# Optimization experiments

Hardware: AMD Instinct MI355X
Metric: run time of the kernel (lower is better)

Reference implementation:

```python
import jax, jax.numpy as jnp
import numpy as np

B, S, D, DFF = 4, 2048, 1024, 4096
EPS = 1e-5


def layernorm(x, g, b):
    mu = jnp.mean(x, axis=-1, keepdims=True)
    var = jnp.mean(jnp.square(x - mu), axis=-1, keepdims=True)
    return (x - mu) * jax.lax.rsqrt(var + EPS) * g + b


def setup_inputs() -> dict:
    key = jax.random.key(0)
    ks = jax.random.split(key, 4)
    hidden_state = jax.random.normal(ks[0], (B, S, D), dtype=jnp.float32)
    attention_mask = jnp.zeros((B, 1, S), dtype=jnp.float32)  # additive mask
    w1 = jax.random.normal(ks[1], (D, DFF), dtype=jnp.float32) * (1.0 / np.sqrt(D))
    b1 = jnp.zeros((DFF,), dtype=jnp.float32)
    w2 = jax.random.normal(ks[2], (DFF, D), dtype=jnp.float32) * (1.0 / np.sqrt(DFF))
    b2 = jnp.zeros((D,), dtype=jnp.float32)
    ln1_g = jnp.ones((D,), dtype=jnp.float32)
    ln1_b = jnp.zeros((D,), dtype=jnp.float32)
    ln2_g = jnp.ones((D,), dtype=jnp.float32)
    ln2_b = jnp.zeros((D,), dtype=jnp.float32)
    return dict(hidden_state=hidden_state, attention_mask=attention_mask,
                w1=w1, b1=b1, w2=w2, b2=b2,
                ln1_g=ln1_g, ln1_b=ln1_b, ln2_g=ln2_g, ln2_b=ln2_b)


def reference(hidden_state, attention_mask, w1, b1, w2, b2, ln1_g, ln1_b, ln2_g, ln2_b):
    x = hidden_state
    d = jnp.asarray(x.shape[-1], x.dtype)
    # hand-rolled single-head attention: q=k=v=x (source forward ignores QKV projections)
    scores = jnp.einsum('bqd,bkd->bqk', x, x) / jnp.sqrt(d) + attention_mask  # [B,S,S]
    attn = jax.nn.softmax(scores, axis=-1)
    attn_out = jnp.einsum('bqk,bkd->bqd', attn, x)
    h = layernorm(x + attn_out, ln1_g, ln1_b)
    # FFN: dense -> exact GELU -> linear_2
    ffn = jnp.einsum('bsf,fd->bsd', jax.nn.gelu(jnp.einsum('bsd,df->bsf', h, w1) + b1, approximate=False), w2) + b2
    return layernorm(h + ffn, ln2_g, ln2_b)
```

## Files before the change

### kernel.cpp

```cpp
#include <hip/hip_runtime.h>
#include <hip/hip_bf16.h>
#include <math.h>

#define LN_EPS 1e-5f

typedef short short8 __attribute__((ext_vector_type(8)));
typedef float floatx4 __attribute__((ext_vector_type(4)));

__device__ inline unsigned short f2bf(float f) {
    unsigned int u = __float_as_uint(f);
    u += 0x7fff + ((u >> 16) & 1);
    return (unsigned short)(u >> 16);
}

__device__ inline void gl_lds16(const unsigned short* g, unsigned short* l) {
    __builtin_amdgcn_global_load_lds(
        (__attribute__((address_space(1))) const void*)g,
        (__attribute__((address_space(3))) void*)l, 16, 0, 0);
}

__device__ inline float gelu_f(float v) {
    float u2 = 2.0f * v * (0.7978845608f + 0.0356774081f * v * v);
    float t  = 1.0f - 2.0f / (__expf(u2) + 1.0f);
    return 0.5f * v * (1.0f + t);
}

#define CFENCE asm volatile("" ::: "memory")

template<int EPI, int BN>
__global__ __launch_bounds__(512, 2) void gemm8p(
    const unsigned short* __restrict__ A, const unsigned short* __restrict__ B,
    const float* __restrict__ bias, const float* __restrict__ resid,
    void* __restrict__ Cptr,
    int M, int N, int K, long sA, long sB, long sC, long sBias, float scale)
{
    static_assert(BN == 256 || BN == 128, "BN must be 256 or 128");
    constexpr int WC = BN / 4;
    constexpr int NT = WC / 16;
    constexpr int NH = NT / 2;

    __shared__ alignas(16) unsigned short lds_a[2][2][256 * 32];
    __shared__ alignas(16) unsigned short lds_b[2][2][BN * 32];

    const int tid  = threadIdx.x;
    const int lane = tid & 63;
    const int wave = tid >> 6;
    const int quad = lane >> 4;
    const int l16  = lane & 15;
    const int wm = wave >> 2;
    const int wn = wave & 3;

    const int nwg = gridDim.x * gridDim.y * gridDim.z;
    int lin = blockIdx.x + gridDim.x * (blockIdx.y + gridDim.y * blockIdx.z);
    if ((nwg & 7) == 0) lin = (lin & 7) * (nwg >> 3) + (lin >> 3);
    const int bx = lin % gridDim.x;
    const int byz = lin / gridDim.x;
    const int by = byz % gridDim.y;
    const int bz = byz / gridDim.y;

    const int tile_m = by * 256;
    const int tile_n = bx * BN;
    const int batch  = bz;

    const unsigned short* Ab = A + (size_t)batch * sA;
    const unsigned short* Bb = B + (size_t)batch * sB;

    const int srow = tid >> 2;
    const int scs  = ((tid & 3) ^ ((tid & 32) ? 2 : 0)) * 8;
    const unsigned short* gA = Ab + (size_t)(tile_m + srow) * K + scs;
    const unsigned short* gB = Bb + (size_t)(tile_n + srow) * K + scs;
    const int ldst = tid * 8;

    const int kcs   = (quad * 8) ^ ((l16 & 8) << 1);
    const int abase = (wm * 128 + l16) * 32 + kcs;
    const int bbase = (wn * WC  + l16) * 32 + kcs;

    floatx4 acc[8][NT];
    const floatx4 zero = {0.f, 0.f, 0.f, 0.f};
#pragma unroll
    for (int i = 0; i < 8; i++)
#pragma unroll
        for (int j = 0; j < NT; j++) acc[i][j] = zero;

    auto stageA = [&](int buf, int h, int k0) {
        const unsigned short* s = gA + (size_t)h * 128 * K + k0;
        gl_lds16(s,      &lds_a[buf][0][h * 4096 + ldst]);
        gl_lds16(s + 32, &lds_a[buf][1][h * 4096 + ldst]);
    };
    auto stageB = [&](int buf, int h, int k0) {
        const unsigned short* s = gB + (size_t)h * 128 * K + k0;
        gl_lds16(s,      &lds_b[buf][0][h * 4096 + ldst]);
        gl_lds16(s + 32, &lds_b[buf][1][h * 4096 + ldst]);
    };

    const int nt = K >> 6;

    stageA(0, 0, 0); stageA(0, 1, 0);
    stageB(0, 0, 0);
    if constexpr (BN == 256) stageB(0, 1, 0);
    if (nt > 1) {
        stageB(1, 0, 64);
        if constexpr (BN == 256) stageB(1, 1, 64);
        if constexpr (BN == 256) { asm volatile("s_waitcnt vmcnt(4)" ::: "memory"); }
        else                     { asm volatile("s_waitcnt vmcnt(2)" ::: "memory"); }
    } else {
        asm volatile("s_waitcnt vmcnt(0)" ::: "memory");
    }
    __builtin_amdgcn_s_barrier(); CFENCE;

    int cur = 0;

    if constexpr (BN == 128) {
        for (int t = 0; t < nt; ++t) {
            const int k0 = t * 64;
            short8 afr[4][2], bfr[2][2];

#pragma unroll
            for (int i = 0; i < 4; i++)
#pragma unroll
                for (int kh = 0; kh < 2; kh++)
                    afr[i][kh] = *(const short8*)&lds_a[cur][kh][abase + i * 512];
#pragma unroll
            for (int j = 0; j < 2; j++)
#pragma unroll
                for (int kh = 0; kh < 2; kh++)
                    bfr[j][kh] = *(const short8*)&lds_b[cur][kh][bbase + j * 512];
            if (t + 1 < nt) { stageA(cur ^ 1, 0, k0 + 64); stageA(cur ^ 1, 1, k0 + 64); }
            CFENCE; __builtin_amdgcn_s_barrier(); CFENCE;
            __builtin_amdgcn_s_setprio(1);
#pragma unroll
            for (int i = 0; i < 4; i++)
#pragma unroll
                for (int j = 0; j < 2; j++)
#pragma unroll
                    for (int kh = 0; kh < 2; kh++)
                        acc[i][j] = __builtin_amdgcn_mfma_f32_16x16x32_bf16(
                            bfr[j][kh], afr[i][kh], acc[i][j], 0, 0, 0);
            __builtin_amdgcn_s_setprio(0);
            CFENCE; __builtin_amdgcn_s_barrier(); CFENCE;

#pragma unroll
            for (int i = 0; i < 4; i++)
#pragma unroll
                for (int kh = 0; kh < 2; kh++)
                    afr[i][kh] = *(const short8*)&lds_a[cur][kh][abase + (4 + i) * 512];
            if (t + 2 < nt) stageB(cur, 0, k0 + 128);
            __builtin_amdgcn_s_setprio(1);
#pragma unroll
            for (int i = 0; i < 4; i++)
#pragma unroll
                for (int j = 0; j < 2; j++)
#pragma unroll
                    for (int kh = 0; kh < 2; kh++)
                        acc[4 + i][j] = __builtin_amdgcn_mfma_f32_16x16x32_bf16(
                            bfr[j][kh], afr[i][kh], acc[4 + i][j], 0, 0, 0);
            __builtin_amdgcn_s_setprio(0);
            if (t + 3 <= nt) {
                asm volatile("s_waitcnt vmcnt(2)" ::: "memory");
                __builtin_amdgcn_s_barrier(); CFENCE;
            } else if (t + 2 == nt) {
                asm volatile("s_waitcnt vmcnt(0)" ::: "memory");
                __builtin_amdgcn_s_barrier(); CFENCE;
            }
            cur ^= 1;
        }
    } else {
        for (int t = 0; t < nt; ++t) {
            const int k0 = t * 64;
            short8 afr[4][2], bfrA[NH][2], bfrB[NH][2];

#pragma unroll
            for (int i = 0; i < 4; i++)
#pragma unroll
                for (int kh = 0; kh < 2; kh++)
                    afr[i][kh] = *(const short8*)&lds_a[cur][kh][abase + i * 512];
#pragma unroll
            for (int j = 0; j < NH; j++)
#pragma unroll
                for (int kh = 0; kh < 2; kh++)
                    bfrA[j][kh] = *(const short8*)&lds_b[cur][kh][bbase + j * 512];
            if (t + 1 < nt) stageA(cur ^ 1, 0, k0 + 64);
            CFENCE; __builtin_amdgcn_s_barrier(); CFENCE;
            __builtin_amdgcn_s_setprio(1);
#pragma unroll
            for (int i = 0; i < 4; i++)
#pragma unroll
                for (int j = 0; j < NH; j++)
#pragma unroll
                    for (int kh = 0; kh < 2; kh++)
                        acc[i][j] = __builtin_amdgcn_mfma_f32_16x16x32_bf16(
                            bfrA[j][kh], afr[i][kh], acc[i][j], 0, 0, 0);
            __builtin_amdgcn_s_setprio(0);
            CFENCE; __builtin_amdgcn_s_barrier(); CFENCE;

#pragma unroll
            for (int j = 0; j < NH; j++)
#pragma unroll
                for (int kh = 0; kh < 2; kh++)
                    bfrB[j][kh] = *(const short8*)&lds_b[cur][kh][bbase + (NH + j) * 512];
            if (t + 1 < nt) stageA(cur ^ 1, 1, k0 + 64);
            CFENCE; __builtin_amdgcn_s_barrier(); CFENCE;
            __builtin_amdgcn_s_setprio(1);
#pragma unroll
            for (int i = 0; i < 4; i++)
#pragma unroll
                for (int j = 0; j < NH; j++)
#pragma unroll
                    for (int kh = 0; kh < 2; kh++)
                        acc[i][NH + j] = __builtin_amdgcn_mfma_f32_16x16x32_bf16(
                            bfrB[j][kh], afr[i][kh], acc[i][NH + j], 0, 0, 0);
            __builtin_amdgcn_s_setprio(0);
            CFENCE; __builtin_amdgcn_s_barrier(); CFENCE;

#pragma unroll
            for (int i = 0; i < 4; i++)
#pragma unroll
                for (int kh = 0; kh < 2; kh++)
                    afr[i][kh] = *(const short8*)&lds_a[cur][kh][abase + (4 + i) * 512];
            if (t + 2 < nt) stageB(cur, 0, k0 + 128);
            CFENCE; __builtin_amdgcn_s_barrier(); CFENCE;
            __builtin_amdgcn_s_setprio(1);
#pragma unroll
            for (int i = 0; i < 4; i++)
#pragma unroll
                for (int j = 0; j < NH; j++)
#pragma unroll
                    for (int kh = 0; kh < 2; kh++)
                        acc[4 + i][NH + j] = __builtin_amdgcn_mfma_f32_16x16x32_bf16(
                            bfrB[j][kh], afr[i][kh], acc[4 + i][NH + j], 0, 0, 0);
            __builtin_amdgcn_s_setprio(0);
            CFENCE; __builtin_amdgcn_s_barrier(); CFENCE;

            if (t + 2 < nt) stageB(cur, 1, k0 + 128);
            __builtin_amdgcn_s_setprio(1);
#pragma unroll
            for (int i = 0; i < 4; i++)
#pragma unroll
                for (int j = 0; j < NH; j++)
#pragma unroll
                    for (int kh = 0; kh < 2; kh++)
                        acc[4 + i][j] = __builtin_amdgcn_mfma_f32_16x16x32_bf16(
                            bfrA[j][kh], afr[i][kh], acc[4 + i][j], 0, 0, 0);
            __builtin_amdgcn_s_setprio(0);
            if (t + 3 <= nt) {
                asm volatile("s_waitcnt vmcnt(4)" ::: "memory");
                __builtin_amdgcn_s_barrier(); CFENCE;
            } else if (t + 2 == nt) {
                asm volatile("s_waitcnt vmcnt(0)" ::: "memory");
                __builtin_amdgcn_s_barrier(); CFENCE;
            }
            cur ^= 1;
        }
    }

#pragma unroll
    for (int i = 0; i < 8; i++) {
        const int row = tile_m + wm * 128 + i * 16 + l16;
#pragma unroll
        for (int j = 0; j < NT; j++) {
            const int colb = tile_n + wn * WC + j * 16 + quad * 4;
            float v[4];
#pragma unroll
            for (int r = 0; r < 4; r++) v[r] = acc[i][j][r];

            if (EPI == 3) {
                float4 mv = *(const float4*)&bias[(size_t)batch * sBias + colb];
                v[0] = v[0] * scale + mv.x;  v[1] = v[1] * scale + mv.y;
                v[2] = v[2] * scale + mv.z;  v[3] = v[3] * scale + mv.w;
            }
            if (EPI == 2 || EPI == 5) {
                float4 bv = *(const float4*)&bias[colb];
                v[0] += bv.x; v[1] += bv.y; v[2] += bv.z; v[3] += bv.w;
            }
            if (EPI == 2) {
#pragma unroll
                for (int r = 0; r < 4; r++) v[r] = gelu_f(v[r]);
            }
            if (EPI == 4 || EPI == 5) {
                float4 rv = *(const float4*)&resid[(size_t)batch * sC +
                                                   (size_t)row * N + colb];
                v[0] += rv.x; v[1] += rv.y; v[2] += rv.z; v[3] += rv.w;
            }

            if (EPI == 2 || EPI == 3) {
                unsigned short* C = (unsigned short*)Cptr + (size_t)batch * sC;
                ushort4 h4;
                h4.x = f2bf(v[0]); h4.y = f2bf(v[1]);
                h4.z = f2bf(v[2]); h4.w = f2bf(v[3]);
                *(ushort4*)(C + (size_t)row * N + colb) = h4;
            } else {
                float* C = (float*)Cptr + (size_t)batch * sC;
                float4 f4 = {v[0], v[1], v[2], v[3]};
                *(float4*)(C + (size_t)row * N + colb) = f4;
            }
        }
    }
}

__global__ __launch_bounds__(256) void x_prep_kernel(
    const float* __restrict__ in, unsigned short* __restrict__ straight,
    unsigned short* __restrict__ transposed, int R, int C, long sIn)
{
    __shared__ float tile[32][33];
    const int tc = blockIdx.x * 32, tr = blockIdx.y * 32;
    const float* src = in + (size_t)blockIdx.z * sIn;
    unsigned short* dstS = straight   + (size_t)blockIdx.z * sIn;
    unsigned short* dstT = transposed + (size_t)blockIdx.z * sIn;
    const int tx = threadIdx.x & 31, ty = threadIdx.x >> 5;
#pragma unroll
    for (int i = 0; i < 4; i++) {
        float val = src[(size_t)(tr + ty + i * 8) * C + tc + tx];
        tile[ty + i * 8][tx] = val;
        dstS[(size_t)(tr + ty + i * 8) * C + tc + tx] = f2bf(val);
    }
    __syncthreads();
#pragma unroll
    for (int i = 0; i < 4; i++)
        dstT[(size_t)(tc + ty + i * 8) * R + tr + tx] = f2bf(tile[tx][ty + i * 8]);
}

__global__ __launch_bounds__(256) void transpose_cvt_kernel(
    const float* __restrict__ in, unsigned short* __restrict__ out, int R, int C)
{
    __shared__ float tile[32][33];
    const int tc = blockIdx.x * 32, tr = blockIdx.y * 32;
    const int tx = threadIdx.x & 31, ty = threadIdx.x >> 5;
#pragma unroll
    for (int i = 0; i < 4; i++)
        tile[ty + i * 8][tx] = in[(size_t)(tr + ty + i * 8) * C + tc + tx];
    __syncthreads();
#pragma unroll
    for (int i = 0; i < 4; i++)
        out[(size_t)(tc + ty + i * 8) * R + tr + tx] = f2bf(tile[tx][ty + i * 8]);
}

__global__ __launch_bounds__(256) void softmax_bf16_kernel(
    const unsigned short* __restrict__ scores, unsigned short* __restrict__ probs,
    int S)
{
    __shared__ float red[4];
    const int row = blockIdx.x;
    const unsigned short* p = scores + (size_t)row * S;
    unsigned short* pr      = probs  + (size_t)row * S;
    const int tid  = threadIdx.x;
    const int lane = tid & 63;
    const int wav  = tid >> 6;

    uint4 raw = *(const uint4*)(p + tid * 8);
    float v[8];
    v[0] = __uint_as_float(raw.x << 16); v[1] = __uint_as_float(raw.x & 0xffff0000u);
    v[2] = __uint_as_float(raw.y << 16); v[3] = __uint_as_float(raw.y & 0xffff0000u);
    v[4] = __uint_as_float(raw.z << 16); v[5] = __uint_as_float(raw.z & 0xffff0000u);
    v[6] = __uint_as_float(raw.w << 16); v[7] = __uint_as_float(raw.w & 0xffff0000u);

    float mx = v[0];
#pragma unroll
    for (int k = 1; k < 8; k++) mx = fmaxf(mx, v[k]);
#pragma unroll
    for (int off = 32; off > 0; off >>= 1) mx = fmaxf(mx, __shfl_down(mx, off));
    if (lane == 0) red[wav] = mx;
    __syncthreads();
    mx = fmaxf(fmaxf(red[0], red[1]), fmaxf(red[2], red[3]));
    __syncthreads();

    float s = 0.f;
#pragma unroll
    for (int k = 0; k < 8; k++) { v[k] = __expf(v[k] - mx); s += v[k]; }
#pragma unroll
    for (int off = 32; off > 0; off >>= 1) s += __shfl_down(s, off);
    if (lane == 0) red[wav] = s;
    __syncthreads();
    s = red[0] + red[1] + red[2] + red[3];
    float inv = 1.0f / s;

    uint4 o;
    o.x = (unsigned)f2bf(v[0] * inv) | ((unsigned)f2bf(v[1] * inv) << 16);
    o.y = (unsigned)f2bf(v[2] * inv) | ((unsigned)f2bf(v[3] * inv) << 16);
    o.z = (unsigned)f2bf(v[4] * inv) | ((unsigned)f2bf(v[5] * inv) << 16);
    o.w = (unsigned)f2bf(v[6] * inv) | ((unsigned)f2bf(v[7] * inv) << 16);
    *(uint4*)(pr + tid * 8) = o;
}

template<int WRITE_BF16>
__global__ __launch_bounds__(256) void ln_kernel(
    const float* __restrict__ X,
    const float* __restrict__ g, const float* __restrict__ bta,
    float* __restrict__ out, unsigned short* __restrict__ out16, int D)
{
    __shared__ float red[8];
    const int row = blockIdx.x;
    const float* x = X + (size_t)row * D;
    const int tid  = threadIdx.x;
    const int lane = tid & 63;
    const int wav  = tid >> 6;

    float4 a = *(const float4*)(x + tid * 4);
    float v0 = a.x, v1 = a.y, v2 = a.z, v3 = a.w;

    float s1 = v0 + v1 + v2 + v3;
    float s2 = v0 * v0 + v1 * v1 + v2 * v2 + v3 * v3;
#pragma unroll
    for (int off = 32; off > 0; off >>= 1) {
        s1 += __shfl_down(s1, off);
        s2 += __shfl_down(s2, off);
    }
    if (lane == 0) { red[wav] = s1; red[4 + wav] = s2; }
    __syncthreads();
    s1 = red[0] + red[1] + red[2] + red[3];
    s2 = red[4] + red[5] + red[6] + red[7];
    const float mu  = s1 / (float)D;
    const float var = s2 / (float)D - mu * mu;
    const float rs  = rsqrtf(var + LN_EPS);

    float4 gg = *(const float4*)(g + tid * 4);
    float4 bb = *(const float4*)(bta + tid * 4);
    float4 r;
    r.x = (v0 - mu) * rs * gg.x + bb.x;
    r.y = (v1 - mu) * rs * gg.y + bb.y;
    r.z = (v2 - mu) * rs * gg.z + bb.z;
    r.w = (v3 - mu) * rs * gg.w + bb.w;
    *(float4*)(out + (size_t)row * D + tid * 4) = r;
    if (WRITE_BF16) {
        ushort4 h;
        h.x = f2bf(r.x); h.y = f2bf(r.y); h.z = f2bf(r.z); h.w = f2bf(r.w);
        *(ushort4*)(out16 + (size_t)row * D + tid * 4) = h;
    }
}

extern "C" void kernel_launch(void* const* d_in, const int* in_sizes, int n_in,
                              void* d_out, int out_size, void* d_ws, size_t ws_size,
                              hipStream_t stream) {
    (void)in_sizes; (void)n_in; (void)out_size; (void)ws_size;
    const float* x    = (const float*)d_in[0];
    const float* mask = (const float*)d_in[1];
    const float* w1   = (const float*)d_in[2];
    const float* b1   = (const float*)d_in[3];
    const float* w2   = (const float*)d_in[4];
    const float* b2   = (const float*)d_in[5];
    const float* ln1g = (const float*)d_in[6];
    const float* ln1b = (const float*)d_in[7];
    const float* ln2g = (const float*)d_in[8];
    const float* ln2b = (const float*)d_in[9];
    float* out = (float*)d_out;

    const int B = 4, S = 2048, D = 1024, DFF = 4096;
    const size_t MB = 1024 * 1024;

    char* ws = (char*)d_ws;
    unsigned short* scoresb = (unsigned short*)ws;
    unsigned short* act     = (unsigned short*)ws;
    unsigned short* xb      = (unsigned short*)(ws + 32 * MB);
    unsigned short* probs   = (unsigned short*)(ws + 32 * MB);
    float*          hbuf    = (float*)(ws + 64 * MB);
    unsigned short* hb16    = (unsigned short*)(ws + 96 * MB);
    unsigned short* w1T     = (unsigned short*)(ws + 112 * MB);
    unsigned short* w2T     = (unsigned short*)(ws + 120 * MB);
    unsigned short* xTb     = (unsigned short*)d_out;
    float*          fsum    = (float*)d_out;

    x_prep_kernel<<<dim3(D / 32, S / 32, B), 256, 0, stream>>>(
        x, xb, xTb, S, D, (long)S * D);
    transpose_cvt_kernel<<<dim3(DFF / 32, D / 32, 1), 256, 0, stream>>>(w1, w1T, D, DFF);
    transpose_cvt_kernel<<<dim3(D / 32, DFF / 32, 1), 256, 0, stream>>>(w2, w2T, DFF, D);

    hipLaunchKernelGGL((gemm8p<3, 256>), dim3(S / 256, S / 256, B), dim3(512), 0, stream,
                       xb, xb, mask, (const float*)nullptr, (void*)scoresb,
                       S, S, D, (long)S * D, (long)S * D, (long)S * S, (long)S, 0.03125f);
    softmax_bf16_kernel<<<B * S, 256, 0, stream>>>(scoresb, probs, S);
    hipLaunchKernelGGL((gemm8p<4, 128>), dim3(D / 128, S / 256, B), dim3(512), 0, stream,
                       probs, xTb, (const float*)nullptr, x, (void*)hbuf,
                       S, D, S, (long)S * S, (long)D * S, (long)S * D, 0L, 0.f);
    hipLaunchKernelGGL((ln_kernel<1>), dim3(B * S), dim3(256), 0, stream,
                       hbuf, ln1g, ln1b, hbuf, hb16, D);
    hipLaunchKernelGGL((gemm8p<2, 256>), dim3(DFF / 256, (B * S) / 256, 1), dim3(512), 0, stream,
                       hb16, w1T, b1, (const float*)nullptr, (void*)act,
                       B * S, DFF, D, 0L, 0L, 0L, 0L, 0.f);
    hipLaunchKernelGGL((gemm8p<5, 256>), dim3(D / 256, (B * S) / 256, 1), dim3(512), 0, stream,
                       act, w2T, b2, hbuf, (void*)fsum,
                       B * S, D, DFF, 0L, 0L, 0L, 0L, 0.f);
    hipLaunchKernelGGL((ln_kernel<0>), dim3(B * S), dim3(256), 0, stream,
                       fsum, ln2g, ln2b, out, (unsigned short*)nullptr, D);
}
```

Before: 455.7 us.

## Add 128x128 GEMM kernel for the N=1024 attention-output and FFN2 GEMMs

Adds a new 256-thread gemm128 kernel with 128x128 tiles and 4 waves, and uses it for the PV GEMM and the FFN second GEMM (N=1024, fp32 output with residual). The grids grow: FFN2 goes from 128 to 512 workgroups and PV from 256 to 512. The aim is better occupancy and load balance across the CUs for these narrow-N GEMMs. gemm8p is reduced to BN=256 with bf16 output only, and the cost is lower per-tile reuse in the new kernel, with more global and LDS traffic per FLOP.

Result: faster. 408.6 us (-10.3%).

```diff
diff --git a/kernel.cpp b/kernel.cpp
--- a/kernel.cpp
+++ b/kernel.cpp
@@ -34,7 +34,7 @@
     void* __restrict__ Cptr,
     int M, int N, int K, long sA, long sB, long sC, long sBias, float scale)
 {
-    static_assert(BN == 256 || BN == 128, "BN must be 256 or 128");
+    static_assert(BN == 256, "gemm8p: BN==256 only (BN=128 -> gemm128)");
     constexpr int WC = BN / 4;
     constexpr int NT = WC / 16;
     constexpr int NH = NT / 2;
@@ -96,161 +96,101 @@
     const int nt = K >> 6;
 
     stageA(0, 0, 0); stageA(0, 1, 0);
-    stageB(0, 0, 0);
-    if constexpr (BN == 256) stageB(0, 1, 0);
+    stageB(0, 0, 0); stageB(0, 1, 0);
     if (nt > 1) {
-        stageB(1, 0, 64);
-        if constexpr (BN == 256) stageB(1, 1, 64);
-        if constexpr (BN == 256) { asm volatile("s_waitcnt vmcnt(4)" ::: "memory"); }
-        else                     { asm volatile("s_waitcnt vmcnt(2)" ::: "memory"); }
+        stageB(1, 0, 64); stageB(1, 1, 64);
+        asm volatile("s_waitcnt vmcnt(4)" ::: "memory");
     } else {
         asm volatile("s_waitcnt vmcnt(0)" ::: "memory");
     }
     __builtin_amdgcn_s_barrier(); CFENCE;
 
     int cur = 0;
-
-    if constexpr (BN == 128) {
-        for (int t = 0; t < nt; ++t) {
-            const int k0 = t * 64;
-            short8 afr[4][2], bfr[2][2];
-
-#pragma unroll
-            for (int i = 0; i < 4; i++)
+    for (int t = 0; t < nt; ++t) {
+        const int k0 = t * 64;
+        short8 afr[4][2], bfrA[NH][2], bfrB[NH][2];
+
+#pragma unroll
+        for (int i = 0; i < 4; i++)
+#pragma unroll
+            for (int kh = 0; kh < 2; kh++)
+                afr[i][kh] = *(const short8*)&lds_a[cur][kh][abase + i * 512];
+#pragma unroll
+        for (int j = 0; j < NH; j++)
+#pragma unroll
+            for (int kh = 0; kh < 2; kh++)
+                bfrA[j][kh] = *(const short8*)&lds_b[cur][kh][bbase + j * 512];
+        if (t + 1 < nt) stageA(cur ^ 1, 0, k0 + 64);
+        CFENCE; __builtin_amdgcn_s_barrier(); CFENCE;
+        __builtin_amdgcn_s_setprio(1);
+#pragma unroll
+        for (int i = 0; i < 4; i++)
+#pragma unroll
+            for (int j = 0; j < NH; j++)
 #pragma unroll
                 for (int kh = 0; kh < 2; kh++)
-                    afr[i][kh] = *(const short8*)&lds_a[cur][kh][abase + i * 512];
-#pragma unroll
-            for (int j = 0; j < 2; j++)
+                    acc[i][j] = __builtin_amdgcn_mfma_f32_16x16x32_bf16(
+                        bfrA[j][kh], afr[i][kh], acc[i][j], 0, 0, 0);
+        __builtin_amdgcn_s_setprio(0);
+        CFENCE; __builtin_amdgcn_s_barrier(); CFENCE;
+
+#pragma unroll
+        for (int j = 0; j < NH; j++)
+#pragma unroll
+            for (int kh = 0; kh < 2; kh++)
+                bfrB[j][kh] = *(const short8*)&lds_b[cur][kh][bbase + (NH + j) * 512];
+        if (t + 1 < nt) stageA(cur ^ 1, 1, k0 + 64);
+        CFENCE; __builtin_amdgcn_s_barrier(); CFENCE;
+        __builtin_amdgcn_s_setprio(1);
+#pragma unroll
+        for (int i = 0; i < 4; i++)
+#pragma unroll
+            for (int j = 0; j < NH; j++)
 #pragma unroll
                 for (int kh = 0; kh < 2; kh++)
-                    bfr[j][kh] = *(const short8*)&lds_b[cur][kh][bbase + j * 512];
-            if (t + 1 < nt) { stageA(cur ^ 1, 0, k0 + 64); stageA(cur ^ 1, 1, k0 + 64); }
-            CFENCE; __builtin_amdgcn_s_barrier(); CFENCE;
-            __builtin_amdgcn_s_setprio(1);
-#pragma unroll
-            for (int i = 0; i < 4; i++)
-#pragma unroll
-                for (int j = 0; j < 2; j++)
-#pragma unroll
-                    for (int kh = 0; kh < 2; kh++)
-                        acc[i][j] = __builtin_amdgcn_mfma_f32_16x16x32_bf16(
-                            bfr[j][kh], afr[i][kh], acc[i][j], 0, 0, 0);
-            __builtin_amdgcn_s_setprio(0);
-            CFENCE; __builtin_amdgcn_s_barrier(); CFENCE;
-
-#pragma unroll
-            for (int i = 0; i < 4; i++)
+                    acc[i][NH + j] = __builtin_amdgcn_mfma_f32_16x16x32_bf16(
+                        bfrB[j][kh], afr[i][kh], acc[i][NH + j], 0, 0, 0);
+        __builtin_amdgcn_s_setprio(0);
+        CFENCE; __builtin_amdgcn_s_barrier(); CFENCE;
+
+#pragma unroll
+        for (int i = 0; i < 4; i++)
+#pragma unroll
+            for (int kh = 0; kh < 2; kh++)
+                afr[i][kh] = *(const short8*)&lds_a[cur][kh][abase + (4 + i) * 512];
+        if (t + 2 < nt) stageB(cur, 0, k0 + 128);
+        CFENCE; __builtin_amdgcn_s_barrier(); CFENCE;
+        __builtin_amdgcn_s_setprio(1);
+#pragma unroll
+        for (int i = 0; i < 4; i++)
+#pragma unroll
+            for (int j = 0; j < NH; j++)
 #pragma unroll
                 for (int kh = 0; kh < 2; kh++)
-                    afr[i][kh] = *(const short8*)&lds_a[cur][kh][abase + (4 + i) * 512];
-            if (t + 2 < nt) stageB(cur, 0, k0 + 128);
-            __builtin_amdgcn_s_setprio(1);
-#pragma unroll
-            for (int i = 0; i < 4; i++)
-#pragma unroll
-                for (int j = 0; j < 2; j++)
-#pragma unroll
-                    for (int kh = 0; kh < 2; kh++)
-                        acc[4 + i][j] = __builtin_amdgcn_mfma_f32_16x16x32_bf16(
-                            bfr[j][kh], afr[i][kh], acc[4 + i][j], 0, 0, 0);
-            __builtin_amdgcn_s_setprio(0);
-            if (t + 3 <= nt) {
-                asm volatile("s_waitcnt vmcnt(2)" ::: "memory");
-                __builtin_amdgcn_s_barrier(); CFENCE;
-            } else if (t + 2 == nt) {
-                asm volatile("s_waitcnt vmcnt(0)" ::: "memory");
-                __builtin_amdgcn_s_barrier(); CFENCE;
-            }
-            cur ^= 1;
+                    acc[4 + i][NH + j] = __builtin_amdgcn_mfma_f32_16x16x32_bf16(
+                        bfrB[j][kh], afr[i][kh], acc[4 + i][NH + j], 0, 0, 0);
+        __builtin_amdgcn_s_setprio(0);
+        CFENCE; __builtin_amdgcn_s_barrier(); CFENCE;
+
+        if (t + 2 < nt) stageB(cur, 1, k0 + 128);
+        __builtin_amdgcn_s_setprio(1);
+#pragma unroll
+        for (int i = 0; i < 4; i++)
+#pragma unroll
+            for (int j = 0; j < NH; j++)
+#pragma unroll
+                for (int kh = 0; kh < 2; kh++)
+                    acc[4 + i][j] = __builtin_amdgcn_mfma_f32_16x16x32_bf16(
+                        bfrA[j][kh], afr[i][kh], acc[4 + i][j], 0, 0, 0);
+        __builtin_amdgcn_s_setprio(0);
+        if (t + 3 <= nt) {
+            asm volatile("s_waitcnt vmcnt(4)" ::: "memory");
+            __builtin_amdgcn_s_barrier(); CFENCE;
+        } else if (t + 2 == nt) {
+            asm volatile("s_waitcnt vmcnt(0)" ::: "memory");
+            __builtin_amdgcn_s_barrier(); CFENCE;
         }
-    } else {
-        for (int t = 0; t < nt; ++t) {
-            const int k0 = t * 64;
-            short8 afr[4][2], bfrA[NH][2], bfrB[NH][2];
-
-#pragma unroll
-            for (int i = 0; i < 4; i++)
-#pragma unroll
-                for (int kh = 0; kh < 2; kh++)
-                    afr[i][kh] = *(const short8*)&lds_a[cur][kh][abase + i * 512];
-#pragma unroll
-            for (int j = 0; j < NH; j++)
-#pragma unroll
-                for (int kh = 0; kh < 2; kh++)
-                    bfrA[j][kh] = *(const short8*)&lds_b[cur][kh][bbase + j * 512];
-            if (t + 1 < nt) stageA(cur ^ 1, 0, k0 + 64);
-            CFENCE; __builtin_amdgcn_s_barrier(); CFENCE;
-            __builtin_amdgcn_s_setprio(1);
-#pragma unroll
-            for (int i = 0; i < 4; i++)
-#pragma unroll
-                for (int j = 0; j < NH; j++)
-#pragma unroll
-                    for (int kh = 0; kh < 2; kh++)
-                        acc[i][j] = __builtin_amdgcn_mfma_f32_16x16x32_bf16(
-                            bfrA[j][kh], afr[i][kh], acc[i][j], 0, 0, 0);
-            __builtin_amdgcn_s_setprio(0);
-            CFENCE; __builtin_amdgcn_s_barrier(); CFENCE;
-
-#pragma unroll
-            for (int j = 0; j < NH; j++)
-#pragma unroll
-                for (int kh = 0; kh < 2; kh++)
-                    bfrB[j][kh] = *(const short8*)&lds_b[cur][kh][bbase + (NH + j) * 512];
-            if (t + 1 < nt) stageA(cur ^ 1, 1, k0 + 64);
-            CFENCE; __builtin_amdgcn_s_barrier(); CFENCE;
-            __builtin_amdgcn_s_setprio(1);
-#pragma unroll
-            for (int i = 0; i < 4; i++)
-#pragma unroll
-                for (int j = 0; j < NH; j++)
-#pragma unroll
-                    for (int kh = 0; kh < 2; kh++)
-                        acc[i][NH + j] = __builtin_amdgcn_mfma_f32_16x16x32_bf16(
-                            bfrB[j][kh], afr[i][kh], acc[i][NH + j], 0, 0, 0);
-            __builtin_amdgcn_s_setprio(0);
-            CFENCE; __builtin_amdgcn_s_barrier(); CFENCE;
-
-#pragma unroll
-            for (int i = 0; i < 4; i++)
-#pragma unroll
-                for (int kh = 0; kh < 2; kh++)
-                    afr[i][kh] = *(const short8*)&lds_a[cur][kh][abase + (4 + i) * 512];
-            if (t + 2 < nt) stageB(cur, 0, k0 + 128);
-            CFENCE; __builtin_amdgcn_s_barrier(); CFENCE;
-            __builtin_amdgcn_s_setprio(1);
-#pragma unroll
-            for (int i = 0; i < 4; i++)
-#pragma unroll
-                for (int j = 0; j < NH; j++)
-#pragma unroll
-                    for (int kh = 0; kh < 2; kh++)
-                        acc[4 + i][NH + j] = __builtin_amdgcn_mfma_f32_16x16x32_bf16(
-                            bfrB[j][kh], afr[i][kh], acc[4 + i][NH + j], 0, 0, 0);
-            __builtin_amdgcn_s_setprio(0);
-            CFENCE; __builtin_amdgcn_s_barrier(); CFENCE;
-
-            if (t + 2 < nt) stageB(cur, 1, k0 + 128);
-            __builtin_amdgcn_s_setprio(1);
-#pragma unroll
-            for (int i = 0; i < 4; i++)
-#pragma unroll
-                for (int j = 0; j < NH; j++)
-#pragma unroll
-                    for (int kh = 0; kh < 2; kh++)
-                        acc[4 + i][j] = __builtin_amdgcn_mfma_f32_16x16x32_bf16(
-                            bfrA[j][kh], afr[i][kh], acc[4 + i][j], 0, 0, 0);
-            __builtin_amdgcn_s_setprio(0);
-            if (t + 3 <= nt) {
-                asm volatile("s_waitcnt vmcnt(4)" ::: "memory");
-                __builtin_amdgcn_s_barrier(); CFENCE;
-            } else if (t + 2 == nt) {
-                asm volatile("s_waitcnt vmcnt(0)" ::: "memory");
-                __builtin_amdgcn_s_barrier(); CFENCE;
-            }
-            cur ^= 1;
-        }
+        cur ^= 1;
     }
 
 #pragma unroll
@@ -268,31 +208,177 @@
                 v[0] = v[0] * scale + mv.x;  v[1] = v[1] * scale + mv.y;
                 v[2] = v[2] * scale + mv.z;  v[3] = v[3] * scale + mv.w;
             }
-            if (EPI == 2 || EPI == 5) {
+            if (EPI == 2) {
+                float4 bv = *(const float4*)&bias[colb];
+                v[0] += bv.x; v[1] += bv.y; v[2] += bv.z; v[3] += bv.w;
+#pragma unroll
+                for (int r = 0; r < 4; r++) v[r] = gelu_f(v[r]);
+            }
+
+            unsigned short* C = (unsigned short*)Cptr + (size_t)batch * sC;
+            ushort4 h4;
+            h4.x = f2bf(v[0]); h4.y = f2bf(v[1]);
+            h4.z = f2bf(v[2]); h4.w = f2bf(v[3]);
+            *(ushort4*)(C + (size_t)row * N + colb) = h4;
+        }
+    }
+}
+
+template<int EPI>
+__global__ __launch_bounds__(256, 2) void gemm128(
+    const unsigned short* __restrict__ A, const unsigned short* __restrict__ B,
+    const float* __restrict__ bias, const float* __restrict__ resid,
+    float* __restrict__ Cptr,
+    int M, int N, int K, long sA, long sB, long sC, float scale)
+{
+    __shared__ alignas(16) unsigned short lds_a[2][2][128 * 32];
+    __shared__ alignas(16) unsigned short lds_b[2][2][128 * 32];
+
+    const int tid  = threadIdx.x;
+    const int lane = tid & 63;
+    const int wave = tid >> 6;
+    const int quad = lane >> 4;
+    const int l16  = lane & 15;
+    const int wm = wave >> 1;
+    const int wn = wave & 1;
+
+    const int nwg = gridDim.x * gridDim.y * gridDim.z;
+    int lin = blockIdx.x + gridDim.x * (blockIdx.y + gridDim.y * blockIdx.z);
+    if ((nwg & 7) == 0) lin = (lin & 7) * (nwg >> 3) + (lin >> 3);
+    const int bx = lin % gridDim.x;
+    const int byz = lin / gridDim.x;
+    const int by = byz % gridDim.y;
+    const int bz = byz / gridDim.y;
+
+    const int tile_m = by * 128;
+    const int tile_n = bx * 128;
+    const int batch  = bz;
+
+    const unsigned short* Ab = A + (size_t)batch * sA;
+    const unsigned short* Bb = B + (size_t)batch * sB;
+
+    const int srow = tid >> 2;
+    const int scs  = ((tid & 3) ^ ((tid & 32) ? 2 : 0)) * 8;
+    const unsigned short* gA = Ab + (size_t)(tile_m + srow) * K + scs;
+    const unsigned short* gB = Bb + (size_t)(tile_n + srow) * K + scs;
+    const int ldst = tid * 8;
+
+    const int kcs   = (quad * 8) ^ ((l16 & 8) << 1);
+    const int abase = (wm * 64 + l16) * 32 + kcs;
+    const int bbase = (wn * 64 + l16) * 32 + kcs;
+
+    floatx4 acc[4][4];
+    const floatx4 zero = {0.f, 0.f, 0.f, 0.f};
+#pragma unroll
+    for (int i = 0; i < 4; i++)
+#pragma unroll
+        for (int j = 0; j < 4; j++) acc[i][j] = zero;
+
+    auto stageA = [&](int buf, int k0) {
+#pragma unroll
+        for (int h = 0; h < 2; h++) {
+            const unsigned short* s = gA + (size_t)h * 64 * K + k0;
+            gl_lds16(s,      &lds_a[buf][0][h * 2048 + ldst]);
+            gl_lds16(s + 32, &lds_a[buf][1][h * 2048 + ldst]);
+        }
+    };
+    auto stageB = [&](int buf, int k0) {
+#pragma unroll
+        for (int h = 0; h < 2; h++) {
+            const unsigned short* s = gB + (size_t)h * 64 * K + k0;
+            gl_lds16(s,      &lds_b[buf][0][h * 2048 + ldst]);
+            gl_lds16(s + 32, &lds_b[buf][1][h * 2048 + ldst]);
+        }
+    };
+
+    const int nt = K >> 6;
+
+    stageA(0, 0);
+    stageB(0, 0);
+    if (nt > 1) {
+        stageB(1, 64);
+        asm volatile("s_waitcnt vmcnt(4)" ::: "memory");
+    } else {
+        asm volatile("s_waitcnt vmcnt(0)" ::: "memory");
+    }
+    __builtin_amdgcn_s_barrier(); CFENCE;
+
+    int cur = 0;
+    for (int t = 0; t < nt; ++t) {
+        const int k0 = t * 64;
+        short8 afr[2][2], bfr[4][2];
+
+#pragma unroll
+        for (int i = 0; i < 2; i++)
+#pragma unroll
+            for (int kh = 0; kh < 2; kh++)
+                afr[i][kh] = *(const short8*)&lds_a[cur][kh][abase + i * 512];
+#pragma unroll
+        for (int j = 0; j < 4; j++)
+#pragma unroll
+            for (int kh = 0; kh < 2; kh++)
+                bfr[j][kh] = *(const short8*)&lds_b[cur][kh][bbase + j * 512];
+        if (t + 1 < nt) stageA(cur ^ 1, k0 + 64);
+        CFENCE; __builtin_amdgcn_s_barrier(); CFENCE;
+        __builtin_amdgcn_s_setprio(1);
+#pragma unroll
+        for (int i = 0; i < 2; i++)
+#pragma unroll
+            for (int j = 0; j < 4; j++)
+#pragma unroll
+                for (int kh = 0; kh < 2; kh++)
+                    acc[i][j] = __builtin_amdgcn_mfma_f32_16x16x32_bf16(
+                        bfr[j][kh], afr[i][kh], acc[i][j], 0, 0, 0);
+        __builtin_amdgcn_s_setprio(0);
+        CFENCE; __builtin_amdgcn_s_barrier(); CFENCE;
+
+#pragma unroll
+        for (int i = 0; i < 2; i++)
+#pragma unroll
+            for (int kh = 0; kh < 2; kh++)
+                afr[i][kh] = *(const short8*)&lds_a[cur][kh][abase + (2 + i) * 512];
+        if (t + 2 < nt) stageB(cur, k0 + 128);
+        __builtin_amdgcn_s_setprio(1);
+#pragma unroll
+        for (int i = 0; i < 2; i++)
+#pragma unroll
+            for (int j = 0; j < 4; j++)
+#pragma unroll
+                for (int kh = 0; kh < 2; kh++)
+                    acc[2 + i][j] = __builtin_amdgcn_mfma_f32_16x16x32_bf16(
+                        bfr[j][kh], afr[i][kh], acc[2 + i][j], 0, 0, 0);
+        __builtin_amdgcn_s_setprio(0);
+        if (t + 3 <= nt) {
+            asm volatile("s_waitcnt vmcnt(4)" ::: "memory");
+            __builtin_amdgcn_s_barrier(); CFENCE;
+        } else if (t + 2 == nt) {
+            asm volatile("s_waitcnt vmcnt(0)" ::: "memory");
+            __builtin_amdgcn_s_barrier(); CFENCE;
+        }
+        cur ^= 1;
+    }
+
+#pragma unroll
+    for (int i = 0; i < 4; i++) {
+        const int row = tile_m + wm * 64 + i * 16 + l16;
+#pragma unroll
+        for (int j = 0; j < 4; j++) {
+            const int colb = tile_n + wn * 64 + j * 16 + quad * 4;
+            float v[4];
+#pragma unroll
+            for (int r = 0; r < 4; r++) v[r] = acc[i][j][r];
+
+            if (EPI == 5) {
                 float4 bv = *(const float4*)&bias[colb];
                 v[0] += bv.x; v[1] += bv.y; v[2] += bv.z; v[3] += bv.w;
             }
-            if (EPI == 2) {
-#pragma unroll
-                for (int r = 0; r < 4; r++) v[r] = gelu_f(v[r]);
-            }
-            if (EPI == 4 || EPI == 5) {
-                float4 rv = *(const float4*)&resid[(size_t)batch * sC +
-                                                   (size_t)row * N + colb];
-                v[0] += rv.x; v[1] += rv.y; v[2] += rv.z; v[3] += rv.w;
-            }
-
-            if (EPI == 2 || EPI == 3) {
-                unsigned short* C = (unsigned short*)Cptr + (size_t)batch * sC;
-                ushort4 h4;
-                h4.x = f2bf(v[0]); h4.y = f2bf(v[1]);
-                h4.z = f2bf(v[2]); h4.w = f2bf(v[3]);
-                *(ushort4*)(C + (size_t)row * N + colb) = h4;
-            } else {
-                float* C = (float*)Cptr + (size_t)batch * sC;
-                float4 f4 = {v[0], v[1], v[2], v[3]};
-                *(float4*)(C + (size_t)row * N + colb) = f4;
-            }
+            float4 rv = *(const float4*)&resid[(size_t)batch * sC +
+                                               (size_t)row * N + colb];
+            v[0] += rv.x; v[1] += rv.y; v[2] += rv.z; v[3] += rv.w;
+
+            float* C = Cptr + (size_t)batch * sC;
+            float4 f4 = {v[0], v[1], v[2], v[3]};
+            *(float4*)(C + (size_t)row * N + colb) = f4;
         }
     }
 }
@@ -467,17 +553,17 @@
                        xb, xb, mask, (const float*)nullptr, (void*)scoresb,
                        S, S, D, (long)S * D, (long)S * D, (long)S * S, (long)S, 0.03125f);
     softmax_bf16_kernel<<<B * S, 256, 0, stream>>>(scoresb, probs, S);
-    hipLaunchKernelGGL((gemm8p<4, 128>), dim3(D / 128, S / 256, B), dim3(512), 0, stream,
-                       probs, xTb, (const float*)nullptr, x, (void*)hbuf,
-                       S, D, S, (long)S * S, (long)D * S, (long)S * D, 0L, 0.f);
+    hipLaunchKernelGGL((gemm128<4>), dim3(D / 128, S / 128, B), dim3(256), 0, stream,
+                       probs, xTb, (const float*)nullptr, x, hbuf,
+                       S, D, S, (long)S * S, (long)D * S, (long)S * D, 0.f);
     hipLaunchKernelGGL((ln_kernel<1>), dim3(B * S), dim3(256), 0, stream,
                        hbuf, ln1g, ln1b, hbuf, hb16, D);
     hipLaunchKernelGGL((gemm8p<2, 256>), dim3(DFF / 256, (B * S) / 256, 1), dim3(512), 0, stream,
                        hb16, w1T, b1, (const float*)nullptr, (void*)act,
                        B * S, DFF, D, 0L, 0L, 0L, 0L, 0.f);
-    hipLaunchKernelGGL((gemm8p<5, 256>), dim3(D / 256, (B * S) / 256, 1), dim3(512), 0, stream,
-                       act, w2T, b2, hbuf, (void*)fsum,
-                       B * S, D, DFF, 0L, 0L, 0L, 0L, 0.f);
+    hipLaunchKernelGGL((gemm128<5>), dim3(D / 128, (B * S) / 128, 1), dim3(256), 0, stream,
+                       act, w2T, b2, hbuf, fsum,
+                       B * S, D, DFF, 0L, 0L, (long)0, 0.f);
     hipLaunchKernelGGL((ln_kernel<0>), dim3(B * S), dim3(256), 0, stream,
                        fsum, ln2g, ln2b, out, (unsigned short*)nullptr, D);
 }
```
